# Kernel tuning notes

Hardware: AMD Instinct MI355X
Metric: run time of the kernel (lower is better)

Reference implementation:

```python
import jax, jax.numpy as jnp
import numpy as np

B, C, H, W = 2, 512, 64, 64


def conv1x1(x, w, b):
    # x: [B,C,H,W], w: [O,C], b: [O]
    return jnp.einsum('bchw,oc->bohw', x, w) + b[None, :, None, None]


def setup_inputs() -> dict:
    key = jax.random.key(0)
    ks = jax.random.split(key, 20)
    d = {
        'visSegF': jax.random.normal(ks[0], (B, C, H, W), jnp.float32),
        'irSegF': jax.random.normal(ks[1], (B, C, H, W), jnp.float32),
        'x_vis_p': jax.random.normal(ks[2], (B, C, H, W), jnp.float32),
        'x_ir_p': jax.random.normal(ks[3], (B, C, H, W), jnp.float32),
    }
    names = ['q_rd', 'k_rd', 'v_rd', 'q_dr', 'k_dr', 'v_dr']
    for i, n in enumerate(names):
        d['W' + n] = jax.random.normal(ks[4 + 2 * i], (C, C), jnp.float32) * 0.02
        d['b' + n] = jax.random.normal(ks[5 + 2 * i], (C,), jnp.float32) * 0.01
    # gamma params are init-zero in torch; use small nonzero values so both paths contribute
    d['gamma_rd'] = jax.random.normal(ks[16], (1,), jnp.float32) * 0.1
    d['gamma_dr'] = jax.random.normal(ks[17], (1,), jnp.float32) * 0.1
    return d


def reference(visSegF, irSegF, x_vis_p, x_ir_p,
              Wq_rd, bq_rd, Wk_rd, bk_rd, Wv_rd, bv_rd,
              Wq_dr, bq_dr, Wk_dr, bk_dr, Wv_dr, bv_dr,
              gamma_rd, gamma_dr):
    b, c, h, w = x_vis_p.shape
    n = h * w

    # rd path: query from x_vis_p, key from visSegF, value from x_ir_p (sr_ratio == 1 branch)
    q_vis = conv1x1(x_vis_p, Wq_rd, bq_rd).reshape(b, c, n)      # [B,C,N]
    key_d = conv1x1(visSegF, Wk_rd, bk_rd).reshape(b, c, -1)     # [B,C,M]
    val_d = conv1x1(x_ir_p, Wv_rd, bv_rd).reshape(b, c, -1)      # [B,C,M]
    # torch: softmax(bmm(q^T, k), dim=1) -> softmax over query positions (axis=1)
    attn_rd = jax.nn.softmax(jnp.einsum('bcn,bcm->bnm', q_vis, key_d), axis=1)
    out_rd = jnp.einsum('bcm,bnm->bcn', val_d, attn_rd).reshape(b, c, h, w)

    # dr path: query from x_ir_p, key/value from irSegF
    q_ir = conv1x1(x_ir_p, Wq_dr, bq_dr).reshape(b, c, n)
    key_r = conv1x1(irSegF, Wk_dr, bk_dr).reshape(b, c, -1)
    val_r = conv1x1(irSegF, Wv_dr, bv_dr).reshape(b, c, -1)
    attn_dr = jax.nn.softmax(jnp.einsum('bcn,bcm->bnm', q_ir, key_r), axis=1)
    out_dr = jnp.einsum('bcm,bnm->bcn', val_r, attn_dr).reshape(b, c, h, w)

    out_rd = jax.nn.relu(gamma_rd[0] * out_rd + x_vis_p)
    out_dr = jax.nn.relu(gamma_dr[0] * out_dr + x_ir_p)
    return (out_rd, out_dr)
```

## Files before the change

### kernel.cpp

```cpp
#include <hip/hip_runtime.h>
#include <stdint.h>


typedef __attribute__((ext_vector_type(8))) __bf16 bf16x8;
typedef __attribute__((ext_vector_type(4))) float f32x4;
typedef __attribute__((ext_vector_type(4))) unsigned short us4;

__device__ __forceinline__ unsigned short f2bf(float f) {
  union { float f; unsigned u; } v; v.f = f;
  unsigned r = v.u + 0x7FFFu + ((v.u >> 16) & 1u);
  return (unsigned short)(r >> 16);
}
__device__ __forceinline__ float bf2f(unsigned short b) {
  union { unsigned u; float f; } v; v.u = ((unsigned)b) << 16;
  return v.f;
}

__device__ __forceinline__ void async_copy16(const unsigned short* g,
                                             unsigned short* l) {
  __builtin_amdgcn_global_load_lds(
      (const __attribute__((address_space(1))) unsigned int*)g,
      (__attribute__((address_space(3))) unsigned int*)l, 16, 0, 0);
}

__device__ __forceinline__ void gemm_core(
    const unsigned short* __restrict__ Ag, const unsigned short* __restrict__ Bg,
    int K, int lda, int ldb, int rowbase, int colbase,
    f32x4 (&acc)[4][4], unsigned short* Al, unsigned short* Bl) {
  const int tid = threadIdx.x;
  const int w = tid >> 6, lane = tid & 63;
  const int quad = lane >> 4, l16 = lane & 15;
  const int wm = (w >> 1) << 6, wn = (w & 1) << 6;
  const int rbase = (w << 5) + (lane >> 2);

  for (int k0 = 0; k0 < K; k0 += 64) {
#pragma unroll
    for (int half = 0; half < 2; ++half) {
      int kh = k0 + (half << 5);
      unsigned short* Ah = Al + (half << 12);
      unsigned short* Bh = Bl + (half << 12);
#pragma unroll
      for (int i = 0; i < 2; ++i) {
        int rloc = rbase + (i << 4);
        int cg = (lane & 3) ^ ((rloc >> 1) & 3);
        int koff = kh + (cg << 3);
        int ldsoff = ((w << 5) + (i << 4)) << 5;
        async_copy16(Ag + (size_t)(rowbase + rloc) * lda + koff, Ah + ldsoff);
        async_copy16(Bg + (size_t)(colbase + rloc) * ldb + koff, Bh + ldsoff);
      }
    }
    __syncthreads();
#pragma unroll
    for (int half = 0; half < 2; ++half) {
      unsigned short* Ah = Al + (half << 12);
      unsigned short* Bh = Bl + (half << 12);
      bf16x8 af[4], bfr[4];
#pragma unroll
      for (int i = 0; i < 4; ++i) {
        int r = wm + (i << 4) + l16;
        af[i] = *(const bf16x8*)(Ah + (r << 5) + ((quad ^ ((r >> 1) & 3)) << 3));
      }
#pragma unroll
      for (int j = 0; j < 4; ++j) {
        int r = wn + (j << 4) + l16;
        bfr[j] = *(const bf16x8*)(Bh + (r << 5) + ((quad ^ ((r >> 1) & 3)) << 3));
      }
#pragma unroll
      for (int i = 0; i < 4; ++i)
#pragma unroll
        for (int j = 0; j < 4; ++j)
          acc[i][j] = __builtin_amdgcn_mfma_f32_16x16x32_bf16(af[i], bfr[j], acc[i][j], 0, 0, 0);
    }
    __syncthreads();
  }
}

struct WArgs { const float* src[6]; unsigned short* dst[6]; };
__global__ __launch_bounds__(256) void k_cvtw(WArgs a) {
  int z = blockIdx.y;
  int i = blockIdx.x * 256 + threadIdx.x;
  a.dst[z][i] = f2bf(a.src[z][i]);
}

struct TArgs { const float* src[4]; unsigned short* dst[4]; };
__global__ __launch_bounds__(256) void k_tcvt(TArgs a) {
  __shared__ float tile[32][33];
  const float* src = a.src[blockIdx.z];
  unsigned short* dst = a.dst[blockIdx.z];
  int n0 = blockIdx.x << 5;
  int r0 = blockIdx.y << 5;
  int tx = threadIdx.x & 31, ty = threadIdx.x >> 5;
#pragma unroll
  for (int i = 0; i < 4; ++i)
    tile[ty * 4 + i][tx] = src[(size_t)(r0 + ty * 4 + i) * 4096 + n0 + tx];
  __syncthreads();
  int b = r0 >> 9, c0 = r0 & 511;
#pragma unroll
  for (int i = 0; i < 4; ++i) {
    int nn = ty * 4 + i;
    dst[(size_t)b * (4096 * 512) + (size_t)(n0 + nn) * 512 + c0 + tx] =
        f2bf(tile[tx][nn]);
  }
}

struct ConvArgs {
  const unsigned short* W[12];
  const unsigned short* X[12];
  const float* bias[12];
  unsigned short* out[12];
  int trans[12];
};
__global__ __launch_bounds__(256) void k_conv(ConvArgs a) {
  __shared__ unsigned short Al[2 * 128 * 32], Bl[2 * 128 * 32];
  int z = blockIdx.z;
  int rowbase = blockIdx.y << 7, colbase = blockIdx.x << 7;
  f32x4 acc[4][4];
#pragma unroll
  for (int i = 0; i < 4; ++i)
#pragma unroll
    for (int j = 0; j < 4; ++j) acc[i][j] = (f32x4){0.f, 0.f, 0.f, 0.f};
  gemm_core(a.W[z], a.X[z], 512, 512, 512, rowbase, colbase, acc, Al, Bl);

  const int tid = threadIdx.x, w = tid >> 6, lane = tid & 63;
  const int quad = lane >> 4, l16 = lane & 15;
  const int wm = (w >> 1) << 6, wn = (w & 1) << 6;
  const float* bias = a.bias[z];
  unsigned short* out = a.out[z];
  if (a.trans[z]) {
#pragma unroll
    for (int i = 0; i < 4; ++i) {
      int o0 = rowbase + wm + (i << 4) + (quad << 2);
      float b0 = bias[o0], b1 = bias[o0 + 1], b2 = bias[o0 + 2], b3 = bias[o0 + 3];
#pragma unroll
      for (int j = 0; j < 4; ++j) {
        int n = colbase + wn + (j << 4) + l16;
        us4 v;
        v.x = f2bf(acc[i][j].x + b0);
        v.y = f2bf(acc[i][j].y + b1);
        v.z = f2bf(acc[i][j].z + b2);
        v.w = f2bf(acc[i][j].w + b3);
        *(us4*)(out + (size_t)n * 512 + o0) = v;
      }
    }
  } else {
#pragma unroll
    for (int i = 0; i < 4; ++i) {
      int o0 = rowbase + wm + (i << 4) + (quad << 2);
      float b0 = bias[o0], b1 = bias[o0 + 1], b2 = bias[o0 + 2], b3 = bias[o0 + 3];
#pragma unroll
      for (int j = 0; j < 4; ++j) {
        int n = colbase + wn + (j << 4) + l16;
        out[(size_t)(o0 + 0) * 4096 + n] = f2bf(acc[i][j].x + b0);
        out[(size_t)(o0 + 1) * 4096 + n] = f2bf(acc[i][j].y + b1);
        out[(size_t)(o0 + 2) * 4096 + n] = f2bf(acc[i][j].z + b2);
        out[(size_t)(o0 + 3) * 4096 + n] = f2bf(acc[i][j].w + b3);
      }
    }
  }
}

struct QKArgs {
  const unsigned short* A[4]; const unsigned short* B[4]; unsigned short* T[4];
  float* pz;
};
__global__ __launch_bounds__(256) void k_qk(QKArgs a) {
  __shared__ unsigned short Al[2 * 128 * 32], Bl[2 * 128 * 32];
  int z = blockIdx.z;
  int rowbase = blockIdx.y << 7;
  int colbase = blockIdx.x << 7;
  f32x4 acc[4][4];
#pragma unroll
  for (int i = 0; i < 4; ++i)
#pragma unroll
    for (int j = 0; j < 4; ++j) acc[i][j] = (f32x4){0.f, 0.f, 0.f, 0.f};
  gemm_core(a.A[z], a.B[z], 512, 512, 512, rowbase, colbase, acc, Al, Bl);

  const int tid = threadIdx.x, w = tid >> 6, lane = tid & 63;
  const int quad = lane >> 4, l16 = lane & 15;
  const int wm = (w >> 1) << 6, wn = (w & 1) << 6;
  unsigned short* T = a.T[z];
  float* red = (float*)Al;
#pragma unroll
  for (int i = 0; i < 4; ++i) {
    int m0 = rowbase + wm + (i << 4) + (quad << 2);
    float rs0 = 0.f, rs1 = 0.f, rs2 = 0.f, rs3 = 0.f;
#pragma unroll
    for (int j = 0; j < 4; ++j) {
      int n = colbase + wn + (j << 4) + l16;
      float e0 = __expf(acc[i][j].x);
      float e1 = __expf(acc[i][j].y);
      float e2 = __expf(acc[i][j].z);
      float e3 = __expf(acc[i][j].w);
      us4 v;
      v.x = f2bf(e0); v.y = f2bf(e1); v.z = f2bf(e2); v.w = f2bf(e3);
      *(us4*)(T + (size_t)n * 4096 + m0) = v;
      rs0 += e0; rs1 += e1; rs2 += e2; rs3 += e3;
    }
#pragma unroll
    for (int d = 1; d < 16; d <<= 1) {
      rs0 += __shfl_xor(rs0, d, 64);
      rs1 += __shfl_xor(rs1, d, 64);
      rs2 += __shfl_xor(rs2, d, 64);
      rs3 += __shfl_xor(rs3, d, 64);
    }
    if (l16 == 0) {
      int lr = (i << 4) + (quad << 2);
      red[(w << 6) + lr + 0] = rs0;
      red[(w << 6) + lr + 1] = rs1;
      red[(w << 6) + lr + 2] = rs2;
      red[(w << 6) + lr + 3] = rs3;
    }
  }
  __syncthreads();
  if (tid < 128) {
    int h = tid >> 6, lr = tid & 63;
    float S = red[((h << 1) << 6) + lr] + red[(((h << 1) + 1) << 6) + lr];
    int m = rowbase + (h << 6) + lr;
    a.pz[((z << 5) + blockIdx.x) * 4096 + m] = S;
  }
}

__global__ __launch_bounds__(256) void k_stats2(const float* __restrict__ pz,
                                                float* __restrict__ c) {
  int m = (blockIdx.x << 8) + threadIdx.x;
  int z = blockIdx.y;
  float S = 0.f;
#pragma unroll
  for (int k = 0; k < 32; ++k) S += pz[((z << 5) + k) * 4096 + m];
  c[z * 4096 + m] = 1.f / S;
}

struct VSArgs { unsigned short* V[4]; const float* c; };
__global__ __launch_bounds__(256) void k_vscale(VSArgs a) {
  int z = blockIdx.y;
  int t = blockIdx.x * 256 + threadIdx.x;
  int m0 = (t & 511) << 3;
  int row = t >> 9;
  unsigned short* p = a.V[z] + (size_t)row * 4096 + m0;
  const float* cz = a.c + z * 4096 + m0;
  int4 raw = *(const int4*)p;
  unsigned short* u = (unsigned short*)&raw;
#pragma unroll
  for (int j = 0; j < 8; ++j) u[j] = f2bf(bf2f(u[j]) * cz[j]);
  *(int4*)p = raw;
}

struct PVArgs {
  const unsigned short* V[4];
  const unsigned short* P[4];
  const float* resid[4];
  const float* gamma[4];
  float* out[4];
};
__global__ __launch_bounds__(256) void k_pv(PVArgs a) {
  __shared__ unsigned short Al[2 * 128 * 32], Bl[2 * 128 * 32];
  int z = blockIdx.z;
  int rowbase = blockIdx.y << 7;
  int colbase = blockIdx.x << 7;
  f32x4 acc[4][4];
#pragma unroll
  for (int i = 0; i < 4; ++i)
#pragma unroll
    for (int j = 0; j < 4; ++j) acc[i][j] = (f32x4){0.f, 0.f, 0.f, 0.f};
  gemm_core(a.V[z], a.P[z], 4096, 4096, 4096, rowbase, colbase, acc, Al, Bl);

  const int tid = threadIdx.x, w = tid >> 6, lane = tid & 63;
  const int quad = lane >> 4, l16 = lane & 15;
  const int wm = (w >> 1) << 6, wn = (w & 1) << 6;
  float g = a.gamma[z][0];
  const float* R = a.resid[z];
  float* O = a.out[z];
#pragma unroll
  for (int i = 0; i < 4; ++i) {
    int c0 = rowbase + wm + (i << 4) + (quad << 2);
#pragma unroll
    for (int j = 0; j < 4; ++j) {
      int n = colbase + wn + (j << 4) + l16;
      O[(size_t)(c0 + 0) * 4096 + n] = fmaxf(g * acc[i][j].x + R[(size_t)(c0 + 0) * 4096 + n], 0.f);
      O[(size_t)(c0 + 1) * 4096 + n] = fmaxf(g * acc[i][j].y + R[(size_t)(c0 + 1) * 4096 + n], 0.f);
      O[(size_t)(c0 + 2) * 4096 + n] = fmaxf(g * acc[i][j].z + R[(size_t)(c0 + 2) * 4096 + n], 0.f);
      O[(size_t)(c0 + 3) * 4096 + n] = fmaxf(g * acc[i][j].w + R[(size_t)(c0 + 3) * 4096 + n], 0.f);
    }
  }
}

extern "C" void kernel_launch(void* const* d_in, const int* in_sizes, int n_in,
                              void* d_out, int out_size, void* d_ws, size_t ws_size,
                              hipStream_t stream) {
  char* ws = (char*)d_ws;
  unsigned short* wb  = (unsigned short*)(ws);
  unsigned short* xt  = (unsigned short*)(ws + 3145728);
  unsigned short* qkv = (unsigned short*)(ws + 36700160);
  unsigned short* tt  = (unsigned short*)(ws + 87031808);
  float* pz  = (float*)(ws + 3145728);
  float* cb  = (float*)(ws + 3145728 + 2097152);

  WArgs wa;
  for (int i = 0; i < 6; ++i) {
    wa.src[i] = (const float*)d_in[4 + 2 * i];
    wa.dst[i] = wb + (size_t)i * 262144;
  }
  k_cvtw<<<dim3(1024, 6), 256, 0, stream>>>(wa);

  TArgs ta;
  for (int ai = 0; ai < 4; ++ai) {
    ta.src[ai] = (const float*)d_in[ai];
    ta.dst[ai] = xt + (size_t)ai * 4194304;
  }
  k_tcvt<<<dim3(128, 32, 4), 256, 0, stream>>>(ta);

  const int srcArr[6] = {2, 0, 3, 3, 1, 1};
  const int trans[6] = {1, 1, 0, 1, 1, 0};
  ConvArgs ca;
  for (int ci = 0; ci < 6; ++ci)
    for (int b = 0; b < 2; ++b) {
      int zz = ci * 2 + b;
      ca.W[zz] = wb + (size_t)ci * 262144;
      ca.X[zz] = xt + (size_t)srcArr[ci] * 4194304 + (size_t)b * 2097152;
      ca.bias[zz] = (const float*)d_in[5 + 2 * ci];
      ca.out[zz] = qkv + (size_t)zz * 2097152;
      ca.trans[zz] = trans[ci];
    }
  k_conv<<<dim3(32, 4, 12), 256, 0, stream>>>(ca);

  QKArgs qa;
  for (int path = 0; path < 2; ++path)
    for (int b = 0; b < 2; ++b) {
      int zz = path * 2 + b;
      qa.A[zz] = qkv + (size_t)((path * 3 + 1) * 2 + b) * 2097152;
      qa.B[zz] = qkv + (size_t)((path * 3 + 0) * 2 + b) * 2097152;
      qa.T[zz] = tt + (size_t)zz * 16777216;
    }
  qa.pz = pz;
  k_qk<<<dim3(32, 32, 4), 256, 0, stream>>>(qa);

  k_stats2<<<dim3(16, 4), 256, 0, stream>>>(pz, cb);

  VSArgs va;
  for (int path = 0; path < 2; ++path)
    for (int b = 0; b < 2; ++b)
      va.V[path * 2 + b] = qkv + (size_t)((path * 3 + 2) * 2 + b) * 2097152;
  va.c = cb;
  k_vscale<<<dim3(1024, 4), 256, 0, stream>>>(va);

  PVArgs pa;
  const float* resid_src[2] = {(const float*)d_in[2], (const float*)d_in[3]};
  const float* gsrc[2] = {(const float*)d_in[16], (const float*)d_in[17]};
  for (int path = 0; path < 2; ++path)
    for (int b = 0; b < 2; ++b) {
      int zz = path * 2 + b;
      pa.V[zz] = qkv + (size_t)((path * 3 + 2) * 2 + b) * 2097152;
      pa.P[zz] = tt + (size_t)zz * 16777216;
      pa.resid[zz] = resid_src[path] + (size_t)b * 2097152;
      pa.gamma[zz] = gsrc[path];
      pa.out[zz] = (float*)d_out + (size_t)path * 4194304 + (size_t)b * 2097152;
    }
  k_pv<<<dim3(32, 4, 4), 256, 0, stream>>>(pa);
}
```

Measured before the change: 424.6 us.

## Stage transposed epilogue stores through LDS and deepen PV k-step

The transposed epilogues of the conv and QK kernels now stage bf16 tiles in shared memory with a padded stride, then write them out as coalesced 16-byte rows instead of scattered 8-byte stores. In QK, the exponentials are computed twice: once for the row-sum reduction and again when writing the tile. The GEMM core is templated on the number of 32-wide k sub-steps, and the PV kernel uses 4 sub-steps (128 k per barrier) with double the LDS. This cuts barrier count in the largest GEMM but may lower occupancy.

New measurement: 438.8 us. 3.4% more time.

```diff
diff --git a/kernel.cpp b/kernel.cpp
--- a/kernel.cpp
+++ b/kernel.cpp
@@ -23,6 +23,7 @@
       (__attribute__((address_space(3))) unsigned int*)l, 16, 0, 0);
 }
 
+template <int NSUB>
 __device__ __forceinline__ void gemm_core(
     const unsigned short* __restrict__ Ag, const unsigned short* __restrict__ Bg,
     int K, int lda, int ldb, int rowbase, int colbase,
@@ -33,9 +34,9 @@
   const int wm = (w >> 1) << 6, wn = (w & 1) << 6;
   const int rbase = (w << 5) + (lane >> 2);
 
-  for (int k0 = 0; k0 < K; k0 += 64) {
-#pragma unroll
-    for (int half = 0; half < 2; ++half) {
+  for (int k0 = 0; k0 < K; k0 += 32 * NSUB) {
+#pragma unroll
+    for (int half = 0; half < NSUB; ++half) {
       int kh = k0 + (half << 5);
       unsigned short* Ah = Al + (half << 12);
       unsigned short* Bh = Bl + (half << 12);
@@ -51,7 +52,7 @@
     }
     __syncthreads();
 #pragma unroll
-    for (int half = 0; half < 2; ++half) {
+    for (int half = 0; half < NSUB; ++half) {
       unsigned short* Ah = Al + (half << 12);
       unsigned short* Bh = Bl + (half << 12);
       bf16x8 af[4], bfr[4];
@@ -111,7 +112,7 @@
   int trans[12];
 };
 __global__ __launch_bounds__(256) void k_conv(ConvArgs a) {
-  __shared__ unsigned short Al[2 * 128 * 32], Bl[2 * 128 * 32];
+  __shared__ unsigned short sh[16384];
   int z = blockIdx.z;
   int rowbase = blockIdx.y << 7, colbase = blockIdx.x << 7;
   f32x4 acc[4][4];
@@ -119,7 +120,7 @@
   for (int i = 0; i < 4; ++i)
 #pragma unroll
     for (int j = 0; j < 4; ++j) acc[i][j] = (f32x4){0.f, 0.f, 0.f, 0.f};
-  gemm_core(a.W[z], a.X[z], 512, 512, 512, rowbase, colbase, acc, Al, Bl);
+  gemm_core<2>(a.W[z], a.X[z], 512, 512, 512, rowbase, colbase, acc, sh, sh + 8192);
 
   const int tid = threadIdx.x, w = tid >> 6, lane = tid & 63;
   const int quad = lane >> 4, l16 = lane & 15;
@@ -128,18 +129,33 @@
   unsigned short* out = a.out[z];
   if (a.trans[z]) {
 #pragma unroll
-    for (int i = 0; i < 4; ++i) {
-      int o0 = rowbase + wm + (i << 4) + (quad << 2);
-      float b0 = bias[o0], b1 = bias[o0 + 1], b2 = bias[o0 + 2], b3 = bias[o0 + 3];
-#pragma unroll
-      for (int j = 0; j < 4; ++j) {
-        int n = colbase + wn + (j << 4) + l16;
-        us4 v;
-        v.x = f2bf(acc[i][j].x + b0);
-        v.y = f2bf(acc[i][j].y + b1);
-        v.z = f2bf(acc[i][j].z + b2);
-        v.w = f2bf(acc[i][j].w + b3);
-        *(us4*)(out + (size_t)n * 512 + o0) = v;
+    for (int p = 0; p < 2; ++p) {
+      __syncthreads();
+      if ((w & 1) == p) {
+#pragma unroll
+        for (int i = 0; i < 4; ++i) {
+          int o_loc = wm + (i << 4) + (quad << 2);
+          int o0 = rowbase + o_loc;
+          float b0 = bias[o0], b1 = bias[o0 + 1], b2 = bias[o0 + 2], b3 = bias[o0 + 3];
+#pragma unroll
+          for (int j = 0; j < 4; ++j) {
+            int n_loc = (j << 4) + l16;
+            us4 v;
+            v.x = f2bf(acc[i][j].x + b0);
+            v.y = f2bf(acc[i][j].y + b1);
+            v.z = f2bf(acc[i][j].z + b2);
+            v.w = f2bf(acc[i][j].w + b3);
+            *(us4*)(sh + n_loc * 136 + o_loc) = v;
+          }
+        }
+      }
+      __syncthreads();
+#pragma unroll
+      for (int q = 0; q < 4; ++q) {
+        int idx = (q << 8) + tid;
+        int row = idx >> 4, chunk = idx & 15;
+        int4 v = *(const int4*)(sh + row * 136 + (chunk << 3));
+        *(int4*)(out + (size_t)(colbase + (p << 6) + row) * 512 + rowbase + (chunk << 3)) = v;
       }
     }
   } else {
@@ -164,7 +180,7 @@
   float* pz;
 };
 __global__ __launch_bounds__(256) void k_qk(QKArgs a) {
-  __shared__ unsigned short Al[2 * 128 * 32], Bl[2 * 128 * 32];
+  __shared__ unsigned short sh[16384];
   int z = blockIdx.z;
   int rowbase = blockIdx.y << 7;
   int colbase = blockIdx.x << 7;
@@ -173,28 +189,22 @@
   for (int i = 0; i < 4; ++i)
 #pragma unroll
     for (int j = 0; j < 4; ++j) acc[i][j] = (f32x4){0.f, 0.f, 0.f, 0.f};
-  gemm_core(a.A[z], a.B[z], 512, 512, 512, rowbase, colbase, acc, Al, Bl);
+  gemm_core<2>(a.A[z], a.B[z], 512, 512, 512, rowbase, colbase, acc, sh, sh + 8192);
 
   const int tid = threadIdx.x, w = tid >> 6, lane = tid & 63;
   const int quad = lane >> 4, l16 = lane & 15;
   const int wm = (w >> 1) << 6, wn = (w & 1) << 6;
   unsigned short* T = a.T[z];
-  float* red = (float*)Al;
+  float* red = (float*)sh;
 #pragma unroll
   for (int i = 0; i < 4; ++i) {
-    int m0 = rowbase + wm + (i << 4) + (quad << 2);
     float rs0 = 0.f, rs1 = 0.f, rs2 = 0.f, rs3 = 0.f;
 #pragma unroll
     for (int j = 0; j < 4; ++j) {
-      int n = colbase + wn + (j << 4) + l16;
-      float e0 = __expf(acc[i][j].x);
-      float e1 = __expf(acc[i][j].y);
-      float e2 = __expf(acc[i][j].z);
-      float e3 = __expf(acc[i][j].w);
-      us4 v;
-      v.x = f2bf(e0); v.y = f2bf(e1); v.z = f2bf(e2); v.w = f2bf(e3);
-      *(us4*)(T + (size_t)n * 4096 + m0) = v;
-      rs0 += e0; rs1 += e1; rs2 += e2; rs3 += e3;
+      rs0 += __expf(acc[i][j].x);
+      rs1 += __expf(acc[i][j].y);
+      rs2 += __expf(acc[i][j].z);
+      rs3 += __expf(acc[i][j].w);
     }
 #pragma unroll
     for (int d = 1; d < 16; d <<= 1) {
@@ -217,6 +227,34 @@
     float S = red[((h << 1) << 6) + lr] + red[(((h << 1) + 1) << 6) + lr];
     int m = rowbase + (h << 6) + lr;
     a.pz[((z << 5) + blockIdx.x) * 4096 + m] = S;
+  }
+#pragma unroll
+  for (int p = 0; p < 2; ++p) {
+    __syncthreads();
+    if ((w & 1) == p) {
+#pragma unroll
+      for (int i = 0; i < 4; ++i) {
+        int m_loc = wm + (i << 4) + (quad << 2);
+#pragma unroll
+        for (int j = 0; j < 4; ++j) {
+          int n_loc = (j << 4) + l16;
+          us4 v;
+          v.x = f2bf(__expf(acc[i][j].x));
+          v.y = f2bf(__expf(acc[i][j].y));
+          v.z = f2bf(__expf(acc[i][j].z));
+          v.w = f2bf(__expf(acc[i][j].w));
+          *(us4*)(sh + n_loc * 136 + m_loc) = v;
+        }
+      }
+    }
+    __syncthreads();
+#pragma unroll
+    for (int q = 0; q < 4; ++q) {
+      int idx = (q << 8) + tid;
+      int row = idx >> 4, chunk = idx & 15;
+      int4 v = *(const int4*)(sh + row * 136 + (chunk << 3));
+      *(int4*)(T + (size_t)(colbase + (p << 6) + row) * 4096 + rowbase + (chunk << 3)) = v;
+    }
   }
 }
 
@@ -253,7 +291,7 @@
   float* out[4];
 };
 __global__ __launch_bounds__(256) void k_pv(PVArgs a) {
-  __shared__ unsigned short Al[2 * 128 * 32], Bl[2 * 128 * 32];
+  __shared__ unsigned short sh[32768];
   int z = blockIdx.z;
   int rowbase = blockIdx.y << 7;
   int colbase = blockIdx.x << 7;
@@ -262,7 +300,7 @@
   for (int i = 0; i < 4; ++i)
 #pragma unroll
     for (int j = 0; j < 4; ++j) acc[i][j] = (f32x4){0.f, 0.f, 0.f, 0.f};
-  gemm_core(a.V[z], a.P[z], 4096, 4096, 4096, rowbase, colbase, acc, Al, Bl);
+  gemm_core<4>(a.V[z], a.P[z], 4096, 4096, 4096, rowbase, colbase, acc, sh, sh + 16384);
 
   const int tid = threadIdx.x, w = tid >> 6, lane = tid & 63;
   const int quad = lane >> 4, l16 = lane & 15;
```

## Swap GEMM operand roles for coalesced stores and deepen PV K-step

Applied to the files above, without the earlier changes.

For the transposed conv outputs and the QK exp tile, the operands are swapped so the MFMA accumulator rows map to the output's strided dimension and the contiguous dimension runs across lanes. Stores become lane-coalesced scalar writes instead of 4-wide scattered vectors. The QK column-sum reduction is reworked to match the new orientation. gemm_core is templated on the number of 32-wide K sub-steps, and the PV GEMM now loads 128 K per barrier using twice the LDS, trading occupancy for fewer syncs.

Result: faster. 399.8 us (-5.8%).

```diff
diff --git a/kernel.cpp b/kernel.cpp
--- a/kernel.cpp
+++ b/kernel.cpp
@@ -4,7 +4,6 @@
 
 typedef __attribute__((ext_vector_type(8))) __bf16 bf16x8;
 typedef __attribute__((ext_vector_type(4))) float f32x4;
-typedef __attribute__((ext_vector_type(4))) unsigned short us4;
 
 __device__ __forceinline__ unsigned short f2bf(float f) {
   union { float f; unsigned u; } v; v.f = f;
@@ -23,6 +22,7 @@
       (__attribute__((address_space(3))) unsigned int*)l, 16, 0, 0);
 }
 
+template <int NSUB>
 __device__ __forceinline__ void gemm_core(
     const unsigned short* __restrict__ Ag, const unsigned short* __restrict__ Bg,
     int K, int lda, int ldb, int rowbase, int colbase,
@@ -33,9 +33,9 @@
   const int wm = (w >> 1) << 6, wn = (w & 1) << 6;
   const int rbase = (w << 5) + (lane >> 2);
 
-  for (int k0 = 0; k0 < K; k0 += 64) {
-#pragma unroll
-    for (int half = 0; half < 2; ++half) {
+  for (int k0 = 0; k0 < K; k0 += 32 * NSUB) {
+#pragma unroll
+    for (int half = 0; half < NSUB; ++half) {
       int kh = k0 + (half << 5);
       unsigned short* Ah = Al + (half << 12);
       unsigned short* Bh = Bl + (half << 12);
@@ -51,7 +51,7 @@
     }
     __syncthreads();
 #pragma unroll
-    for (int half = 0; half < 2; ++half) {
+    for (int half = 0; half < NSUB; ++half) {
       unsigned short* Ah = Al + (half << 12);
       unsigned short* Bh = Bl + (half << 12);
       bf16x8 af[4], bfr[4];
@@ -111,35 +111,39 @@
   int trans[12];
 };
 __global__ __launch_bounds__(256) void k_conv(ConvArgs a) {
-  __shared__ unsigned short Al[2 * 128 * 32], Bl[2 * 128 * 32];
+  __shared__ unsigned short sh[16384];
   int z = blockIdx.z;
-  int rowbase = blockIdx.y << 7, colbase = blockIdx.x << 7;
+  int trans = a.trans[z];
+  int rowbase = (trans ? blockIdx.x : blockIdx.y) << 7;
+  int colbase = (trans ? blockIdx.y : blockIdx.x) << 7;
+  const unsigned short* Ag = trans ? a.X[z] : a.W[z];
+  const unsigned short* Bg = trans ? a.W[z] : a.X[z];
   f32x4 acc[4][4];
 #pragma unroll
   for (int i = 0; i < 4; ++i)
 #pragma unroll
     for (int j = 0; j < 4; ++j) acc[i][j] = (f32x4){0.f, 0.f, 0.f, 0.f};
-  gemm_core(a.W[z], a.X[z], 512, 512, 512, rowbase, colbase, acc, Al, Bl);
+  gemm_core<2>(Ag, Bg, 512, 512, 512, rowbase, colbase, acc, sh, sh + 8192);
 
   const int tid = threadIdx.x, w = tid >> 6, lane = tid & 63;
   const int quad = lane >> 4, l16 = lane & 15;
   const int wm = (w >> 1) << 6, wn = (w & 1) << 6;
   const float* bias = a.bias[z];
   unsigned short* out = a.out[z];
-  if (a.trans[z]) {
+  if (trans) {
+    float bo[4];
+#pragma unroll
+    for (int j = 0; j < 4; ++j) bo[j] = bias[colbase + wn + (j << 4) + l16];
 #pragma unroll
     for (int i = 0; i < 4; ++i) {
-      int o0 = rowbase + wm + (i << 4) + (quad << 2);
-      float b0 = bias[o0], b1 = bias[o0 + 1], b2 = bias[o0 + 2], b3 = bias[o0 + 3];
+      int n0 = rowbase + wm + (i << 4) + (quad << 2);
 #pragma unroll
       for (int j = 0; j < 4; ++j) {
-        int n = colbase + wn + (j << 4) + l16;
-        us4 v;
-        v.x = f2bf(acc[i][j].x + b0);
-        v.y = f2bf(acc[i][j].y + b1);
-        v.z = f2bf(acc[i][j].z + b2);
-        v.w = f2bf(acc[i][j].w + b3);
-        *(us4*)(out + (size_t)n * 512 + o0) = v;
+        int o = colbase + wn + (j << 4) + l16;
+        out[(size_t)(n0 + 0) * 512 + o] = f2bf(acc[i][j].x + bo[j]);
+        out[(size_t)(n0 + 1) * 512 + o] = f2bf(acc[i][j].y + bo[j]);
+        out[(size_t)(n0 + 2) * 512 + o] = f2bf(acc[i][j].z + bo[j]);
+        out[(size_t)(n0 + 3) * 512 + o] = f2bf(acc[i][j].w + bo[j]);
       }
     }
   } else {
@@ -160,63 +164,57 @@
 }
 
 struct QKArgs {
-  const unsigned short* A[4]; const unsigned short* B[4]; unsigned short* T[4];
+  const unsigned short* Q[4]; const unsigned short* K[4]; unsigned short* T[4];
   float* pz;
 };
 __global__ __launch_bounds__(256) void k_qk(QKArgs a) {
-  __shared__ unsigned short Al[2 * 128 * 32], Bl[2 * 128 * 32];
+  __shared__ unsigned short sh[16384];
   int z = blockIdx.z;
-  int rowbase = blockIdx.y << 7;
-  int colbase = blockIdx.x << 7;
+  int nbase = blockIdx.y << 7;
+  int mbase = blockIdx.x << 7;
   f32x4 acc[4][4];
 #pragma unroll
   for (int i = 0; i < 4; ++i)
 #pragma unroll
     for (int j = 0; j < 4; ++j) acc[i][j] = (f32x4){0.f, 0.f, 0.f, 0.f};
-  gemm_core(a.A[z], a.B[z], 512, 512, 512, rowbase, colbase, acc, Al, Bl);
+  gemm_core<2>(a.Q[z], a.K[z], 512, 512, 512, nbase, mbase, acc, sh, sh + 8192);
 
   const int tid = threadIdx.x, w = tid >> 6, lane = tid & 63;
   const int quad = lane >> 4, l16 = lane & 15;
   const int wm = (w >> 1) << 6, wn = (w & 1) << 6;
   unsigned short* T = a.T[z];
-  float* red = (float*)Al;
+  float sjv[4] = {0.f, 0.f, 0.f, 0.f};
 #pragma unroll
   for (int i = 0; i < 4; ++i) {
-    int m0 = rowbase + wm + (i << 4) + (quad << 2);
-    float rs0 = 0.f, rs1 = 0.f, rs2 = 0.f, rs3 = 0.f;
+    int n0 = nbase + wm + (i << 4) + (quad << 2);
 #pragma unroll
     for (int j = 0; j < 4; ++j) {
-      int n = colbase + wn + (j << 4) + l16;
+      int m = mbase + wn + (j << 4) + l16;
       float e0 = __expf(acc[i][j].x);
       float e1 = __expf(acc[i][j].y);
       float e2 = __expf(acc[i][j].z);
       float e3 = __expf(acc[i][j].w);
-      us4 v;
-      v.x = f2bf(e0); v.y = f2bf(e1); v.z = f2bf(e2); v.w = f2bf(e3);
-      *(us4*)(T + (size_t)n * 4096 + m0) = v;
-      rs0 += e0; rs1 += e1; rs2 += e2; rs3 += e3;
-    }
-#pragma unroll
-    for (int d = 1; d < 16; d <<= 1) {
-      rs0 += __shfl_xor(rs0, d, 64);
-      rs1 += __shfl_xor(rs1, d, 64);
-      rs2 += __shfl_xor(rs2, d, 64);
-      rs3 += __shfl_xor(rs3, d, 64);
-    }
-    if (l16 == 0) {
-      int lr = (i << 4) + (quad << 2);
-      red[(w << 6) + lr + 0] = rs0;
-      red[(w << 6) + lr + 1] = rs1;
-      red[(w << 6) + lr + 2] = rs2;
-      red[(w << 6) + lr + 3] = rs3;
-    }
+      T[(size_t)(n0 + 0) * 4096 + m] = f2bf(e0);
+      T[(size_t)(n0 + 1) * 4096 + m] = f2bf(e1);
+      T[(size_t)(n0 + 2) * 4096 + m] = f2bf(e2);
+      T[(size_t)(n0 + 3) * 4096 + m] = f2bf(e3);
+      sjv[j] += e0 + e1 + e2 + e3;
+    }
+  }
+  float* red = (float*)sh;
+#pragma unroll
+  for (int j = 0; j < 4; ++j) {
+    float s = sjv[j];
+    s += __shfl_xor(s, 16, 64);
+    s += __shfl_xor(s, 32, 64);
+    if (quad == 0) red[(w << 6) + (j << 4) + l16] = s;
   }
   __syncthreads();
   if (tid < 128) {
-    int h = tid >> 6, lr = tid & 63;
-    float S = red[((h << 1) << 6) + lr] + red[(((h << 1) + 1) << 6) + lr];
-    int m = rowbase + (h << 6) + lr;
-    a.pz[((z << 5) + blockIdx.x) * 4096 + m] = S;
+    int h = tid >> 6, t = tid & 63;
+    float S = red[(h << 6) + t] + red[((h + 2) << 6) + t];
+    int m = mbase + (h << 6) + t;
+    a.pz[((z << 5) + blockIdx.y) * 4096 + m] = S;
   }
 }
 
@@ -253,7 +251,7 @@
   float* out[4];
 };
 __global__ __launch_bounds__(256) void k_pv(PVArgs a) {
-  __shared__ unsigned short Al[2 * 128 * 32], Bl[2 * 128 * 32];
+  __shared__ unsigned short sh[32768];
   int z = blockIdx.z;
   int rowbase = blockIdx.y << 7;
   int colbase = blockIdx.x << 7;
@@ -262,7 +260,7 @@
   for (int i = 0; i < 4; ++i)
 #pragma unroll
     for (int j = 0; j < 4; ++j) acc[i][j] = (f32x4){0.f, 0.f, 0.f, 0.f};
-  gemm_core(a.V[z], a.P[z], 4096, 4096, 4096, rowbase, colbase, acc, Al, Bl);
+  gemm_core<4>(a.V[z], a.P[z], 4096, 4096, 4096, rowbase, colbase, acc, sh, sh + 16384);
 
   const int tid = threadIdx.x, w = tid >> 6, lane = tid & 63;
   const int quad = lane >> 4, l16 = lane & 15;
@@ -327,8 +325,8 @@
   for (int path = 0; path < 2; ++path)
     for (int b = 0; b < 2; ++b) {
       int zz = path * 2 + b;
-      qa.A[zz] = qkv + (size_t)((path * 3 + 1) * 2 + b) * 2097152;
-      qa.B[zz] = qkv + (size_t)((path * 3 + 0) * 2 + b) * 2097152;
+      qa.Q[zz] = qkv + (size_t)((path * 3 + 0) * 2 + b) * 2097152;
+      qa.K[zz] = qkv + (size_t)((path * 3 + 1) * 2 + b) * 2097152;
       qa.T[zz] = tt + (size_t)zz * 16777216;
     }
   qa.pz = pz;
```
